# Performance work log

Measured on AMD Instinct MI355X. Metric: run time of the kernel, lower is better.

## Reference

```python
import jax, jax.numpy as jnp
import numpy as np

D_MODEL = 1024
HEADS = 16
D_K = D_MODEL // HEADS
B, S = 4, 2048


def setup_inputs() -> dict:
    key = jax.random.key(0)
    ks = jax.random.split(key, 12)
    xav = float(np.sqrt(6.0 / (D_MODEL + D_MODEL)))  # xavier_uniform bound
    inp = {
        "query": jax.random.normal(ks[0], (B, S, D_MODEL), jnp.float32),
        "key": jax.random.normal(ks[1], (B, S, D_MODEL), jnp.float32),
        "value": jax.random.normal(ks[2], (B, S, D_MODEL), jnp.float32),
        # causal mask, broadcast over batch and heads: [1,1,S,S]
        "mask": jnp.tril(jnp.ones((S, S), jnp.int32))[None, None],
        "Wq": jax.random.uniform(ks[3], (D_MODEL, D_MODEL), jnp.float32, -xav, xav),
        "bq": jnp.zeros((D_MODEL,), jnp.float32),
        "Wk": jax.random.uniform(ks[4], (D_MODEL, D_MODEL), jnp.float32, -xav, xav),
        "bk": jnp.zeros((D_MODEL,), jnp.float32),
        "Wv": jax.random.uniform(ks[5], (D_MODEL, D_MODEL), jnp.float32, -xav, xav),
        "bv": jnp.zeros((D_MODEL,), jnp.float32),
        "Wo": jax.random.uniform(ks[6], (D_MODEL, D_MODEL), jnp.float32, -xav, xav),
        "bo": jnp.zeros((D_MODEL,), jnp.float32),
    }
    return inp


def reference(query, key, value, mask, Wq, bq, Wk, bk, Wv, bv, Wo, bo):
    b, s, d = query.shape
    # torch Linear: y = x @ W.T + b, W is [out, in]
    Q = (jnp.einsum("bsd,ed->bse", query, Wq) + bq).reshape(b, s, HEADS, D_K).transpose(0, 2, 1, 3)
    K = (jnp.einsum("bsd,ed->bse", key, Wk) + bk).reshape(b, -1, HEADS, D_K).transpose(0, 2, 1, 3)
    V = (jnp.einsum("bsd,ed->bse", value, Wv) + bv).reshape(b, -1, HEADS, D_K).transpose(0, 2, 1, 3)
    scale = 1.0 / jnp.sqrt(jnp.asarray(D_K, query.dtype))
    scores = jnp.einsum("bhqd,bhkd->bhqk", Q, K) * scale  # [B,H,S,S]
    scores = jnp.where(mask == 0, -jnp.inf, scores)
    attn = jax.nn.softmax(scores, axis=-1)
    attn = jnp.where(jnp.isnan(attn), jnp.zeros_like(attn), attn)  # nan-fix as in source
    out = jnp.einsum("bhqk,bhkd->bhqd", attn, V)
    out = out.transpose(0, 2, 1, 3).reshape(b, s, d)
    return jnp.einsum("bsd,ed->bse", out, Wo) + bo
```

## Files before the change

kernel.cpp:

```cpp
#include <hip/hip_runtime.h>
#include <hip/hip_bf16.h>

#define DM 1024
#define NHEADS 16
#define DKH 64
#define BATCH 4
#define SEQ 2048
#define MROWS (BATCH*SEQ)

typedef __attribute__((ext_vector_type(8))) short bf16x8;
typedef __attribute__((ext_vector_type(4))) short bf16x4;
typedef __attribute__((ext_vector_type(4))) float f32x4;

__device__ __forceinline__ unsigned short f2bf(float f){
  unsigned u = __float_as_uint(f);
  u += 0x7fffu + ((u >> 16) & 1u);
  return (unsigned short)(u >> 16);
}

__device__ __forceinline__ void gload16(const unsigned short* g, unsigned short* l){
  __builtin_amdgcn_global_load_lds((const __attribute__((address_space(1))) void*)g,
                                   (__attribute__((address_space(3))) void*)l, 16, 0, 0);
}

__global__ __launch_bounds__(256) void conv_f32_bf16(const float* __restrict__ in,
                                                     unsigned short* __restrict__ out, int n){
  int i = (blockIdx.x * blockDim.x + threadIdx.x) * 4;
  if (i < n){
    const float4 v = *reinterpret_cast<const float4*>(in + i);
    ushort4 o;
    o.x = f2bf(v.x); o.y = f2bf(v.y); o.z = f2bf(v.z); o.w = f2bf(v.w);
    *reinterpret_cast<ushort4*>(out + i) = o;
  }
}

template<int MODE>
__global__ __launch_bounds__(256)
void gemm_bt(const unsigned short* __restrict__ A, const unsigned short* __restrict__ Bw,
             const float* __restrict__ bias, void* __restrict__ out, float scale)
{
  const int K = 1024;
  __shared__ short a_sh[128*64];
  __shared__ short b_sh[128*64];
  const int tid  = threadIdx.x;
  const int lane = tid & 63;
  const int wid  = tid >> 6;
  const int wm = wid >> 1, wn = wid & 1;
  const int tileM = blockIdx.x * 128;
  const int tileN = blockIdx.y * 128;

  f32x4 acc[4][4];
  #pragma unroll
  for (int i = 0; i < 4; i++)
    #pragma unroll
    for (int j = 0; j < 4; j++)
      acc[i][j] = (f32x4){0.f,0.f,0.f,0.f};

  const int lr = lane & 15;
  const int lg = lane >> 4;

  for (int k0 = 0; k0 < K; k0 += 64){
    bf16x8 ra[4], rb[4];
    #pragma unroll
    for (int i = 0; i < 4; i++){
      int v   = tid + 256*i;
      int row = v >> 3;
      int cg  = v & 7;
      ra[i] = *reinterpret_cast<const bf16x8*>(A  + (size_t)(tileM+row)*K + k0 + cg*8);
      rb[i] = *reinterpret_cast<const bf16x8*>(Bw + (size_t)(tileN+row)*K + k0 + cg*8);
    }
    __syncthreads();
    #pragma unroll
    for (int i = 0; i < 4; i++){
      int v   = tid + 256*i;
      int row = v >> 3;
      int cg  = v & 7;
      *reinterpret_cast<bf16x8*>(&a_sh[row*64 + ((cg ^ (row & 7)) * 8)]) = ra[i];
      *reinterpret_cast<bf16x8*>(&b_sh[row*64 + ((cg ^ (row & 7)) * 8)]) = rb[i];
    }
    __syncthreads();
    #pragma unroll
    for (int kk = 0; kk < 64; kk += 32){
      bf16x8 af[4], bfr[4];
      const int g0 = lg + (kk >> 3);
      #pragma unroll
      for (int fm = 0; fm < 4; fm++){
        int row = wm*64 + fm*16 + lr;
        af[fm] = *reinterpret_cast<const bf16x8*>(&a_sh[row*64 + ((g0 ^ (row & 7)) * 8)]);
      }
      #pragma unroll
      for (int fn = 0; fn < 4; fn++){
        int row = wn*64 + fn*16 + lr;
        bfr[fn] = *reinterpret_cast<const bf16x8*>(&b_sh[row*64 + ((g0 ^ (row & 7)) * 8)]);
      }
      #pragma unroll
      for (int fm = 0; fm < 4; fm++)
        #pragma unroll
        for (int fn = 0; fn < 4; fn++)
          acc[fm][fn] = __builtin_amdgcn_mfma_f32_16x16x32_bf16(af[fm], bfr[fn], acc[fm][fn], 0, 0, 0);
    }
  }

  #pragma unroll
  for (int fm = 0; fm < 4; fm++){
    #pragma unroll
    for (int fn = 0; fn < 4; fn++){
      #pragma unroll
      for (int r = 0; r < 4; r++){
        int m = tileM + wm*64 + fm*16 + lg*4 + r;
        int n = tileN + wn*64 + fn*16 + lr;
        float val = acc[fm][fn][r] + bias[n];
        if (MODE == 0){
          val *= scale;
          int b = m >> 11, s = m & 2047, h = n >> 6, d = n & 63;
          ((unsigned short*)out)[(((size_t)(b*NHEADS + h)*SEQ + s)*DKH + d)] = f2bf(val);
        } else if (MODE == 1){
          int b = m >> 11, s = m & 2047, h = n >> 6, d = n & 63;
          ((unsigned short*)out)[(((size_t)(b*NHEADS + h)*DKH + d)*SEQ + s)] = f2bf(val);
        } else {
          ((float*)out)[(size_t)m*DM + n] = val;
        }
      }
    }
  }
}

__global__ __launch_bounds__(256)
void attn_kernel(const unsigned short* __restrict__ Q, const unsigned short* __restrict__ Kb,
                 const unsigned short* __restrict__ Vt, unsigned short* __restrict__ Oout)
{
  __shared__ unsigned short k_sh[2][64*64];
  __shared__ unsigned short v_sh[2][64*64];
  const int lane = threadIdx.x & 63;
  const int w    = threadIdx.x >> 6;
  const int lr = lane & 15, grp = lane >> 4;
  const int bh = blockIdx.x;
  const int qtile = 15 - (int)blockIdx.y;
  const int qb0 = qtile * 128;
  const int qw0 = qb0 + w * 32;
  const int b = bh >> 4, h = bh & 15;
  const size_t kbase = (size_t)bh * SEQ * DKH;
  const size_t vbase = (size_t)bh * DKH * SEQ;

  const int r8 = lane >> 3, c8 = lane & 7;
  const int rowS0 = w*16 + r8;
  const int rowS1 = w*16 + 8 + r8;
  const size_t offK0 = (size_t)rowS0*DKH  + (size_t)((c8 ^ (rowS0 & 7)) * 8);
  const size_t offK1 = (size_t)rowS1*DKH  + (size_t)((c8 ^ (rowS1 & 7)) * 8);
  const size_t offV0 = (size_t)rowS0*SEQ  + (size_t)((c8 ^ (rowS0 & 7)) * 8);
  const size_t offV1 = (size_t)rowS1*SEQ  + (size_t)((c8 ^ (rowS1 & 7)) * 8);
  const int ldsA = (w*16)*64;
  const int ldsB = (w*16+8)*64;

  bf16x8 qf[2][2];
  #pragma unroll
  for (int qg = 0; qg < 2; qg++){
    size_t off = kbase + (size_t)(qw0 + qg*16 + lr)*DKH + grp*8;
    qf[qg][0] = *reinterpret_cast<const bf16x8*>(Q + off);
    qf[qg][1] = *reinterpret_cast<const bf16x8*>(Q + off + 32);
  }

  float mrun[2] = {-__builtin_inff(), -__builtin_inff()};
  float lrun[2] = {0.f, 0.f};
  f32x4 o[2][4];
  #pragma unroll
  for (int qg = 0; qg < 2; qg++)
    #pragma unroll
    for (int dc = 0; dc < 4; dc++) o[qg][dc] = (f32x4){0.f,0.f,0.f,0.f};

  const int nkb = qb0/64 + 2;

#define STAGE(kb_, bf_) do { \
    gload16(Kb + kbase + (size_t)(kb_)*4096 + offK0, (unsigned short*)&k_sh[bf_][ldsA]); \
    gload16(Kb + kbase + (size_t)(kb_)*4096 + offK1, (unsigned short*)&k_sh[bf_][ldsB]); \
    gload16(Vt + vbase + (size_t)(kb_)*64   + offV0, (unsigned short*)&v_sh[bf_][ldsA]); \
    gload16(Vt + vbase + (size_t)(kb_)*64   + offV1, (unsigned short*)&v_sh[bf_][ldsB]); \
  } while(0)

  STAGE(0, 0);
  __syncthreads();

  for (int kb = 0; kb < nkb; kb++){
    const int buf = kb & 1;
    if (kb + 1 < nkb) STAGE(kb + 1, buf ^ 1);

    if (kb*64 <= qw0 + 31){
      const unsigned short* ks = k_sh[buf];
      const unsigned short* vs = v_sh[buf];
      const bool act0 = (kb*64 <= qw0 + 15);

      f32x4 st[2][4];
      #pragma unroll
      for (int ksub = 0; ksub < 4; ksub++){
        int rowk = ksub*16 + lr;
        bf16x8 kf0 = *reinterpret_cast<const bf16x8*>(&ks[rowk*64 + ((grp ^ (rowk & 7)) * 8)]);
        bf16x8 kf1 = *reinterpret_cast<const bf16x8*>(&ks[rowk*64 + (((4 + grp) ^ (rowk & 7)) * 8)]);
        #pragma unroll
        for (int qg = 0; qg < 2; qg++){
          f32x4 s = (f32x4){0.f,0.f,0.f,0.f};
          s = __builtin_amdgcn_mfma_f32_16x16x32_bf16(kf0, qf[qg][0], s, 0, 0, 0);
          s = __builtin_amdgcn_mfma_f32_16x16x32_bf16(kf1, qf[qg][1], s, 0, 0, 0);
          st[qg][ksub] = s;
        }
      }

      bf16x4 pb[2][4];
      #pragma unroll
      for (int qg = 0; qg < 2; qg++){
        if (qg == 0 && !act0) continue;
        const int qgb = qw0 + qg*16;
        if (kb*64 + 63 > qgb){
          #pragma unroll
          for (int ksub = 0; ksub < 4; ksub++)
            #pragma unroll
            for (int r = 0; r < 4; r++){
              int kg = kb*64 + ksub*16 + grp*4 + r;
              if (kg > qgb + lr) st[qg][ksub][r] = -__builtin_inff();
            }
        }
        float mt = st[qg][0][0];
        #pragma unroll
        for (int ksub = 0; ksub < 4; ksub++)
          #pragma unroll
          for (int r = 0; r < 4; r++) mt = fmaxf(mt, st[qg][ksub][r]);
        mt = fmaxf(mt, __shfl_xor(mt, 16));
        mt = fmaxf(mt, __shfl_xor(mt, 32));
        float mnew = fmaxf(mrun[qg], mt);
        float corr = __expf(mrun[qg] - mnew);
        float ps = 0.f;
        #pragma unroll
        for (int ksub = 0; ksub < 4; ksub++){
          #pragma unroll
          for (int r = 0; r < 4; r++){
            float p = __expf(st[qg][ksub][r] - mnew);
            ps += p;
            pb[qg][ksub][r] = (short)f2bf(p);
          }
        }
        ps += __shfl_xor(ps, 16);
        ps += __shfl_xor(ps, 32);
        lrun[qg] = lrun[qg]*corr + ps;
        mrun[qg] = mnew;
        #pragma unroll
        for (int dc = 0; dc < 4; dc++){
          o[qg][dc][0] *= corr; o[qg][dc][1] *= corr;
          o[qg][dc][2] *= corr; o[qg][dc][3] *= corr;
        }
      }

      #pragma unroll
      for (int ksub = 0; ksub < 4; ksub++){
        #pragma unroll
        for (int dc = 0; dc < 4; dc++){
          int rowd = dc*16 + lr;
          int cg16 = ksub*2 + (grp >> 1);
          bf16x4 vf = *reinterpret_cast<const bf16x4*>(
              &vs[rowd*64 + ((cg16 ^ (rowd & 7)) * 8) + (grp & 1)*4]);
          if (act0) o[0][dc] = __builtin_amdgcn_mfma_f32_16x16x16bf16_1k(vf, pb[0][ksub], o[0][dc], 0, 0, 0);
          o[1][dc] = __builtin_amdgcn_mfma_f32_16x16x16bf16_1k(vf, pb[1][ksub], o[1][dc], 0, 0, 0);
        }
      }
    }
    __syncthreads();
  }
#undef STAGE

  #pragma unroll
  for (int qg = 0; qg < 2; qg++){
    float inv = 1.0f / lrun[qg];
    int qglob = qw0 + qg*16 + lr;
    size_t ob = ((size_t)(b*SEQ + qglob))*DM + h*DKH;
    #pragma unroll
    for (int dc = 0; dc < 4; dc++){
      ushort4 pk;
      pk.x = f2bf(o[qg][dc][0]*inv);
      pk.y = f2bf(o[qg][dc][1]*inv);
      pk.z = f2bf(o[qg][dc][2]*inv);
      pk.w = f2bf(o[qg][dc][3]*inv);
      *reinterpret_cast<ushort4*>(&Oout[ob + dc*16 + grp*4]) = pk;
    }
  }
}

extern "C" void kernel_launch(void* const* d_in, const int* in_sizes, int n_in,
                              void* d_out, int out_size, void* d_ws, size_t ws_size,
                              hipStream_t stream) {
  const float* query = (const float*)d_in[0];
  const float* key   = (const float*)d_in[1];
  const float* value = (const float*)d_in[2];
  const float* Wq = (const float*)d_in[4];
  const float* bq = (const float*)d_in[5];
  const float* Wk = (const float*)d_in[6];
  const float* bk = (const float*)d_in[7];
  const float* Wv = (const float*)d_in[8];
  const float* bv = (const float*)d_in[9];
  const float* Wo = (const float*)d_in[10];
  const float* bo = (const float*)d_in[11];
  float* out = (float*)d_out;

  char* ws = (char*)d_ws;
  const size_t SZ_X = (size_t)MROWS * DM * 2;
  const size_t SZ_W = (size_t)DM * DM * 2;
  unsigned short* qb  = (unsigned short*)(ws + 0);
  unsigned short* kb  = (unsigned short*)(ws + SZ_X);
  unsigned short* vb  = (unsigned short*)(ws + 2*SZ_X);
  unsigned short* wqb = (unsigned short*)(ws + 3*SZ_X);
  unsigned short* wkb = (unsigned short*)(ws + 3*SZ_X + SZ_W);
  unsigned short* wvb = (unsigned short*)(ws + 3*SZ_X + 2*SZ_W);
  unsigned short* wob = (unsigned short*)(ws + 3*SZ_X + 3*SZ_W);
  unsigned short* Vt  = (unsigned short*)(ws + 3*SZ_X + 4*SZ_W);
  unsigned short* Qb   = vb;
  unsigned short* Kbuf = qb;
  unsigned short* attO = kb;

  const int nX = MROWS * DM;
  const int nW = DM * DM;
  conv_f32_bf16<<<nX/1024, 256, 0, stream>>>(query, qb, nX);
  conv_f32_bf16<<<nX/1024, 256, 0, stream>>>(key,   kb, nX);
  conv_f32_bf16<<<nX/1024, 256, 0, stream>>>(value, vb, nX);
  conv_f32_bf16<<<nW/1024, 256, 0, stream>>>(Wq, wqb, nW);
  conv_f32_bf16<<<nW/1024, 256, 0, stream>>>(Wk, wkb, nW);
  conv_f32_bf16<<<nW/1024, 256, 0, stream>>>(Wv, wvb, nW);
  conv_f32_bf16<<<nW/1024, 256, 0, stream>>>(Wo, wob, nW);

  dim3 gg(MROWS/128, DM/128);
  gemm_bt<1><<<gg, 256, 0, stream>>>(vb, wvb, bv, (void*)Vt,   1.0f);
  gemm_bt<0><<<gg, 256, 0, stream>>>(qb, wqb, bq, (void*)Qb,   0.125f);
  gemm_bt<0><<<gg, 256, 0, stream>>>(kb, wkb, bk, (void*)Kbuf, 1.0f);

  attn_kernel<<<dim3(64, 16), 256, 0, stream>>>(Qb, Kbuf, Vt, attO);

  gemm_bt<2><<<gg, 256, 0, stream>>>(attO, wob, bo, (void*)out, 1.0f);
}
```

Measured before the change: 221.1 us.

## Fuse conversion launches, use exp2 softmax, compute row sums via MFMA, add setprio

Merges the seven f32-to-bf16 conversion launches into one kernel that dispatches by block index. Folds log2(e) into the Q projection scale so softmax uses the native exp2, and replaces the shuffle-based row-sum reduction with an extra MFMA against a ones vector. It also tree-reduces the row max and raises wave priority around the MFMA sections. The goal is lower launch overhead and less VALU/shuffle work in attention, at the cost of extra MFMA instructions and row sums built from bf16-rounded probabilities.

```diff
diff --git a/kernel.cpp b/kernel.cpp
--- a/kernel.cpp
+++ b/kernel.cpp
@@ -12,6 +12,12 @@
 typedef __attribute__((ext_vector_type(4))) short bf16x4;
 typedef __attribute__((ext_vector_type(4))) float f32x4;
 
+#if __has_builtin(__builtin_amdgcn_exp2f)
+#define EXP2(x) __builtin_amdgcn_exp2f(x)
+#else
+#define EXP2(x) exp2f(x)
+#endif
+
 __device__ __forceinline__ unsigned short f2bf(float f){
   unsigned u = __float_as_uint(f);
   u += 0x7fffu + ((u >> 16) & 1u);
@@ -23,15 +29,20 @@
                                    (__attribute__((address_space(3))) void*)l, 16, 0, 0);
 }
 
-__global__ __launch_bounds__(256) void conv_f32_bf16(const float* __restrict__ in,
-                                                     unsigned short* __restrict__ out, int n){
-  int i = (blockIdx.x * blockDim.x + threadIdx.x) * 4;
-  if (i < n){
-    const float4 v = *reinterpret_cast<const float4*>(in + i);
-    ushort4 o;
-    o.x = f2bf(v.x); o.y = f2bf(v.y); o.z = f2bf(v.z); o.w = f2bf(v.w);
-    *reinterpret_cast<ushort4*>(out + i) = o;
-  }
+struct ConvArgs { const float* src[7]; unsigned short* dst[7]; };
+
+__global__ __launch_bounds__(256) void conv_all(ConvArgs a){
+  const int bx = blockIdx.x;
+  int t, boff;
+  if (bx < 24576){ t = bx >> 13; boff = bx & 8191; }
+  else { int j = bx - 24576; t = 3 + (j >> 10); boff = j & 1023; }
+  const float* __restrict__ src = a.src[t];
+  unsigned short* __restrict__ dst = a.dst[t];
+  const int i = (boff * 256 + threadIdx.x) * 4;
+  const float4 v = *reinterpret_cast<const float4*>(src + i);
+  ushort4 o;
+  o.x = f2bf(v.x); o.y = f2bf(v.y); o.z = f2bf(v.z); o.w = f2bf(v.w);
+  *reinterpret_cast<ushort4*>(dst + i) = o;
 }
 
 template<int MODE>
@@ -160,13 +171,19 @@
     qf[qg][1] = *reinterpret_cast<const bf16x8*>(Q + off + 32);
   }
 
+  bf16x4 ones4;
+  ones4[0] = (short)0x3F80; ones4[1] = (short)0x3F80;
+  ones4[2] = (short)0x3F80; ones4[3] = (short)0x3F80;
+
   float mrun[2] = {-__builtin_inff(), -__builtin_inff()};
-  float lrun[2] = {0.f, 0.f};
+  f32x4 ls[2];
   f32x4 o[2][4];
   #pragma unroll
-  for (int qg = 0; qg < 2; qg++)
+  for (int qg = 0; qg < 2; qg++){
+    ls[qg] = (f32x4){0.f,0.f,0.f,0.f};
     #pragma unroll
     for (int dc = 0; dc < 4; dc++) o[qg][dc] = (f32x4){0.f,0.f,0.f,0.f};
+  }
 
   const int nkb = qb0/64 + 2;
 
@@ -190,6 +207,7 @@
       const bool act0 = (kb*64 <= qw0 + 15);
 
       f32x4 st[2][4];
+      __builtin_amdgcn_s_setprio(1);
       #pragma unroll
       for (int ksub = 0; ksub < 4; ksub++){
         int rowk = ksub*16 + lr;
@@ -203,6 +221,7 @@
           st[qg][ksub] = s;
         }
       }
+      __builtin_amdgcn_s_setprio(0);
 
       bf16x4 pb[2][4];
       #pragma unroll
@@ -218,36 +237,37 @@
               if (kg > qgb + lr) st[qg][ksub][r] = -__builtin_inff();
             }
         }
-        float mt = st[qg][0][0];
-        #pragma unroll
-        for (int ksub = 0; ksub < 4; ksub++)
-          #pragma unroll
-          for (int r = 0; r < 4; r++) mt = fmaxf(mt, st[qg][ksub][r]);
+        float mt = fmaxf(fmaxf(st[qg][0][0], st[qg][0][1]), fmaxf(st[qg][0][2], st[qg][0][3]));
+        #pragma unroll
+        for (int ksub = 1; ksub < 4; ksub++){
+          mt = fmaxf(mt, fmaxf(fmaxf(st[qg][ksub][0], st[qg][ksub][1]),
+                               fmaxf(st[qg][ksub][2], st[qg][ksub][3])));
+        }
         mt = fmaxf(mt, __shfl_xor(mt, 16));
         mt = fmaxf(mt, __shfl_xor(mt, 32));
-        float mnew = fmaxf(mrun[qg], mt);
-        float corr = __expf(mrun[qg] - mnew);
-        float ps = 0.f;
-        #pragma unroll
-        for (int ksub = 0; ksub < 4; ksub++){
-          #pragma unroll
-          for (int r = 0; r < 4; r++){
-            float p = __expf(st[qg][ksub][r] - mnew);
-            ps += p;
-            pb[qg][ksub][r] = (short)f2bf(p);
-          }
-        }
-        ps += __shfl_xor(ps, 16);
-        ps += __shfl_xor(ps, 32);
-        lrun[qg] = lrun[qg]*corr + ps;
+        const float mnew = fmaxf(mrun[qg], mt);
+        const float corr = EXP2(mrun[qg] - mnew);
         mrun[qg] = mnew;
         #pragma unroll
         for (int dc = 0; dc < 4; dc++){
           o[qg][dc][0] *= corr; o[qg][dc][1] *= corr;
           o[qg][dc][2] *= corr; o[qg][dc][3] *= corr;
         }
-      }
-
+        ls[qg][0] *= corr;
+        #pragma unroll
+        for (int ksub = 0; ksub < 4; ksub++){
+          float p0 = EXP2(st[qg][ksub][0] - mnew);
+          float p1 = EXP2(st[qg][ksub][1] - mnew);
+          float p2 = EXP2(st[qg][ksub][2] - mnew);
+          float p3 = EXP2(st[qg][ksub][3] - mnew);
+          pb[qg][ksub][0] = (short)f2bf(p0);
+          pb[qg][ksub][1] = (short)f2bf(p1);
+          pb[qg][ksub][2] = (short)f2bf(p2);
+          pb[qg][ksub][3] = (short)f2bf(p3);
+        }
+      }
+
+      __builtin_amdgcn_s_setprio(1);
       #pragma unroll
       for (int ksub = 0; ksub < 4; ksub++){
         #pragma unroll
@@ -259,7 +279,10 @@
           if (act0) o[0][dc] = __builtin_amdgcn_mfma_f32_16x16x16bf16_1k(vf, pb[0][ksub], o[0][dc], 0, 0, 0);
           o[1][dc] = __builtin_amdgcn_mfma_f32_16x16x16bf16_1k(vf, pb[1][ksub], o[1][dc], 0, 0, 0);
         }
-      }
+        if (act0) ls[0] = __builtin_amdgcn_mfma_f32_16x16x16bf16_1k(ones4, pb[0][ksub], ls[0], 0, 0, 0);
+        ls[1] = __builtin_amdgcn_mfma_f32_16x16x16bf16_1k(ones4, pb[1][ksub], ls[1], 0, 0, 0);
+      }
+      __builtin_amdgcn_s_setprio(0);
     }
     __syncthreads();
   }
@@ -267,7 +290,7 @@
 
   #pragma unroll
   for (int qg = 0; qg < 2; qg++){
-    float inv = 1.0f / lrun[qg];
+    float inv = 1.0f / ls[qg][0];
     int qglob = qw0 + qg*16 + lr;
     size_t ob = ((size_t)(b*SEQ + qglob))*DM + h*DKH;
     #pragma unroll
@@ -313,19 +336,17 @@
   unsigned short* Kbuf = qb;
   unsigned short* attO = kb;
 
-  const int nX = MROWS * DM;
-  const int nW = DM * DM;
-  conv_f32_bf16<<<nX/1024, 256, 0, stream>>>(query, qb, nX);
-  conv_f32_bf16<<<nX/1024, 256, 0, stream>>>(key,   kb, nX);
-  conv_f32_bf16<<<nX/1024, 256, 0, stream>>>(value, vb, nX);
-  conv_f32_bf16<<<nW/1024, 256, 0, stream>>>(Wq, wqb, nW);
-  conv_f32_bf16<<<nW/1024, 256, 0, stream>>>(Wk, wkb, nW);
-  conv_f32_bf16<<<nW/1024, 256, 0, stream>>>(Wv, wvb, nW);
-  conv_f32_bf16<<<nW/1024, 256, 0, stream>>>(Wo, wob, nW);
+  ConvArgs ca;
+  ca.src[0] = query; ca.src[1] = key; ca.src[2] = value;
+  ca.src[3] = Wq; ca.src[4] = Wk; ca.src[5] = Wv; ca.src[6] = Wo;
+  ca.dst[0] = qb; ca.dst[1] = kb; ca.dst[2] = vb;
+  ca.dst[3] = wqb; ca.dst[4] = wkb; ca.dst[5] = wvb; ca.dst[6] = wob;
+  conv_all<<<28672, 256, 0, stream>>>(ca);
 
   dim3 gg(MROWS/128, DM/128);
+  const float qscale = 0.125f * 1.4426950408889634f;
   gemm_bt<1><<<gg, 256, 0, stream>>>(vb, wvb, bv, (void*)Vt,   1.0f);
-  gemm_bt<0><<<gg, 256, 0, stream>>>(qb, wqb, bq, (void*)Qb,   0.125f);
+  gemm_bt<0><<<gg, 256, 0, stream>>>(qb, wqb, bq, (void*)Qb,   qscale);
   gemm_bt<0><<<gg, 256, 0, stream>>>(kb, wkb, bk, (void*)Kbuf, 1.0f);
 
   attn_kernel<<<dim3(64, 16), 256, 0, stream>>>(Qb, Kbuf, Vt, attO);
```

New measurement: 216.6 us. 2.0% less time.
